# Kernel tuning notes

Measured on AMD Instinct MI355X. Metric: run time of the kernel, lower is better.

Reference implementation:

```python
import jax, jax.numpy as jnp
import numpy as np

T, D_IN, N_RES, D_OUT = 8192, 64, 2048, 64
SPECTRAL_RADIUS = 0.95


def setup_inputs() -> dict:
    key = jax.random.key(0)
    k1, k2, k3, k4, k5 = jax.random.split(key, 5)
    u = jax.random.normal(k1, (T, D_IN), dtype=jnp.float32)
    W_in = jax.random.normal(k2, (N_RES, D_IN), dtype=jnp.float32) * 0.1
    W = jax.random.normal(k3, (N_RES, N_RES), dtype=jnp.float32)
    # Spectral-radius rescale exactly as in __init__: max |Re(eigvals)|
    max_eig = float(np.max(np.abs(np.linalg.eigvals(np.asarray(W)).real)))
    W = W * (SPECTRAL_RADIUS / max_eig)
    W_out = jax.random.normal(k4, (D_OUT, N_RES), dtype=jnp.float32) * (1.0 / np.sqrt(N_RES))
    b_out = jax.random.normal(k5, (D_OUT,), dtype=jnp.float32) * 0.01
    return {"u": u, "W_in": W_in, "W": W, "W_out": W_out, "b_out": b_out}


def reference(u, W_in, W, W_out, b_out):
    # x_t = tanh(W_in @ u_t + W @ x_{t-1}); y_t = W_out @ x_t + b
    # Precompute input projections for all timesteps in one GEMM.
    inp_proj = u @ W_in.T  # (T, N_RES)

    def step(x, proj_t):
        x_new = jnp.tanh(proj_t + W @ x)
        return x_new, x_new

    x0 = jnp.zeros((N_RES,), dtype=u.dtype)
    _, states = jax.lax.scan(step, x0, inp_proj)  # states: (T, N_RES)
    outputs = states @ W_out.T + b_out            # (T, D_OUT)
    return outputs
```

## Files before the change

kernel.cpp:

```cpp
#include <hip/hip_runtime.h>

#define T_STEPS 8192
#define NRES    2048
#define DIN     64
#define DOUT    64

typedef unsigned long long u64;
typedef unsigned int u32;


__global__ __launch_bounds__(256) void esn_init_ring(u64* __restrict__ ring) {
  int idx = blockIdx.x * 256 + threadIdx.x;
  if (idx < 3 * NRES) ring[idx] = 0ull;
}

__global__ __launch_bounds__(256) void esn_transpose(const float* __restrict__ Wout,
                                                     float* __restrict__ WT) {
  int idx = blockIdx.x * 256 + threadIdx.x;
  int d = idx >> 11;
  int k = idx & (NRES - 1);
  WT[k * DOUT + d] = Wout[idx];
}

__global__ __launch_bounds__(256) void esn_scan(const float* __restrict__ u,
                                                const float* __restrict__ Win,
                                                const float* __restrict__ W,
                                                float* __restrict__ states,
                                                u64* __restrict__ ring) {
  const int tid  = threadIdx.x;
  const int lane = tid & 63;
  const int wv   = tid >> 6;
  const int blk  = blockIdx.x;
  const int r0   = blk * 8 + wv * 2;
  const int r1   = r0 + 1;

  __shared__ float xs[NRES];

  float w0[32], w1[32];
#pragma unroll
  for (int g = 0; g < 8; ++g) {
    const float4 a = *(const float4*)(W + (size_t)r0 * NRES + g * 256 + lane * 4);
    w0[g * 4 + 0] = a.x; w0[g * 4 + 1] = a.y; w0[g * 4 + 2] = a.z; w0[g * 4 + 3] = a.w;
    const float4 c = *(const float4*)(W + (size_t)r1 * NRES + g * 256 + lane * 4);
    w1[g * 4 + 0] = c.x; w1[g * 4 + 1] = c.y; w1[g * 4 + 2] = c.z; w1[g * 4 + 3] = c.w;
  }
  const float win0 = Win[r0 * DIN + lane];
  const float win1 = Win[r1 * DIN + lane];

  for (int t = 0; t < T_STEPS; ++t) {
    __syncthreads();
    if (t == 0) {
#pragma unroll
      for (int j = 0; j < 8; ++j) xs[j * 256 + tid] = 0.0f;
    } else {
      const u64* rb  = ring + ((t + 2) % 3) * NRES;
      const u32 want = (u32)t;
      u64 v[8];
#pragma unroll
      for (int j = 0; j < 8; ++j)
        v[j] = __hip_atomic_load(rb + j * 256 + tid, __ATOMIC_RELAXED,
                                 __HIP_MEMORY_SCOPE_AGENT);
      for (;;) {
        bool ok = true;
#pragma unroll
        for (int j = 0; j < 8; ++j) ok = ok && ((u32)v[j] == want);
        if (ok) break;
#pragma unroll
        for (int j = 0; j < 8; ++j)
          if ((u32)v[j] != want)
            v[j] = __hip_atomic_load(rb + j * 256 + tid, __ATOMIC_RELAXED,
                                     __HIP_MEMORY_SCOPE_AGENT);
      }
#pragma unroll
      for (int j = 0; j < 8; ++j)
        xs[j * 256 + tid] = __uint_as_float((u32)(v[j] >> 32));
    }
    __syncthreads();

    const float uv = u[t * DIN + lane];
    float a0 = win0 * uv;
    float a1 = win1 * uv;
#pragma unroll
    for (int g = 0; g < 8; ++g) {
      const float4 xv = *(const float4*)(xs + g * 256 + lane * 4);
      a0 = fmaf(w0[g * 4 + 0], xv.x, a0);
      a0 = fmaf(w0[g * 4 + 1], xv.y, a0);
      a0 = fmaf(w0[g * 4 + 2], xv.z, a0);
      a0 = fmaf(w0[g * 4 + 3], xv.w, a0);
      a1 = fmaf(w1[g * 4 + 0], xv.x, a1);
      a1 = fmaf(w1[g * 4 + 1], xv.y, a1);
      a1 = fmaf(w1[g * 4 + 2], xv.z, a1);
      a1 = fmaf(w1[g * 4 + 3], xv.w, a1);
    }
#pragma unroll
    for (int off = 32; off > 0; off >>= 1) {
      a0 += __shfl_xor(a0, off, 64);
      a1 += __shfl_xor(a1, off, 64);
    }
    if (lane < 2) {
      const float s  = (lane == 0) ? a0 : a1;
      const float xv = tanhf(s);
      const int r    = r0 + lane;
      states[(size_t)t * NRES + r] = xv;
      const u64 word = ((u64)__float_as_uint(xv) << 32) | (u32)(t + 1);
      __hip_atomic_store(ring + (t % 3) * NRES + r, word, __ATOMIC_RELAXED,
                         __HIP_MEMORY_SCOPE_AGENT);
    }
  }
}

__global__ __launch_bounds__(256) void esn_out_gemm(const float* __restrict__ states,
                                                    const float* __restrict__ WT,
                                                    const float* __restrict__ bout,
                                                    float* __restrict__ out) {
  const int tid  = threadIdx.x;
  const int lane = tid & 63;
  const int grp  = tid >> 6;
  const int t0   = blockIdx.x * 16 + grp * 4;

  float acc0 = 0.f, acc1 = 0.f, acc2 = 0.f, acc3 = 0.f;
  const float* s0 = states + (size_t)(t0 + 0) * NRES;
  const float* s1 = states + (size_t)(t0 + 1) * NRES;
  const float* s2 = states + (size_t)(t0 + 2) * NRES;
  const float* s3 = states + (size_t)(t0 + 3) * NRES;

  for (int k = 0; k < NRES; k += 4) {
    const float4 a = *(const float4*)(s0 + k);
    const float4 b = *(const float4*)(s1 + k);
    const float4 c = *(const float4*)(s2 + k);
    const float4 d = *(const float4*)(s3 + k);
    const float wA = WT[(k + 0) * DOUT + lane];
    const float wB = WT[(k + 1) * DOUT + lane];
    const float wC = WT[(k + 2) * DOUT + lane];
    const float wD = WT[(k + 3) * DOUT + lane];
    acc0 = fmaf(a.x, wA, acc0); acc0 = fmaf(a.y, wB, acc0);
    acc0 = fmaf(a.z, wC, acc0); acc0 = fmaf(a.w, wD, acc0);
    acc1 = fmaf(b.x, wA, acc1); acc1 = fmaf(b.y, wB, acc1);
    acc1 = fmaf(b.z, wC, acc1); acc1 = fmaf(b.w, wD, acc1);
    acc2 = fmaf(c.x, wA, acc2); acc2 = fmaf(c.y, wB, acc2);
    acc2 = fmaf(c.z, wC, acc2); acc2 = fmaf(c.w, wD, acc2);
    acc3 = fmaf(d.x, wA, acc3); acc3 = fmaf(d.y, wB, acc3);
    acc3 = fmaf(d.z, wC, acc3); acc3 = fmaf(d.w, wD, acc3);
  }
  const float bb = bout[lane];
  out[(size_t)(t0 + 0) * DOUT + lane] = acc0 + bb;
  out[(size_t)(t0 + 1) * DOUT + lane] = acc1 + bb;
  out[(size_t)(t0 + 2) * DOUT + lane] = acc2 + bb;
  out[(size_t)(t0 + 3) * DOUT + lane] = acc3 + bb;
}

extern "C" void kernel_launch(void* const* d_in, const int* in_sizes, int n_in,
                              void* d_out, int out_size, void* d_ws, size_t ws_size,
                              hipStream_t stream) {
  const float* u    = (const float*)d_in[0];
  const float* Win  = (const float*)d_in[1];
  const float* W    = (const float*)d_in[2];
  const float* Wout = (const float*)d_in[3];
  const float* bout = (const float*)d_in[4];
  float* out = (float*)d_out;

  char* ws = (char*)d_ws;
  float* states = (float*)ws;
  u64*   ring   = (u64*)(ws + (size_t)T_STEPS * NRES * sizeof(float));
  float* WT     = (float*)(ws + (size_t)T_STEPS * NRES * sizeof(float)
                              + (size_t)3 * NRES * sizeof(u64));

  hipLaunchKernelGGL(esn_init_ring, dim3(24), dim3(256), 0, stream, ring);
  hipLaunchKernelGGL(esn_transpose, dim3((DOUT * NRES) / 256), dim3(256), 0, stream,
                     Wout, WT);
  hipLaunchKernelGGL(esn_scan, dim3(256), dim3(256), 0, stream,
                     u, Win, W, states, ring);
  hipLaunchKernelGGL(esn_out_gemm, dim3(T_STEPS / 16), dim3(256), 0, stream,
                     states, WT, bout, out);
}
```

Measured before the change: 23.40 ms.

## Pack two state values per ring word using NaN sentinels instead of step tags

Changes the cross-block handoff ring from one value plus a step tag per 64-bit word to two float values per word. A quiet-NaN pattern marks empty slots, and a 4-deep ring lets each producer clear the slot for a future step after writing. This halves the number of atomic loads each thread polls per step and the volume of synchronisation traffic. The u load is also hoisted ahead of the spin loop. It relies on tanh never producing NaN and on the clear-ahead ordering staying correct with relaxed atomics.

```diff
diff --git a/kernel.cpp b/kernel.cpp
--- a/kernel.cpp
+++ b/kernel.cpp
@@ -8,10 +8,12 @@
 typedef unsigned long long u64;
 typedef unsigned int u32;
 
+#define QNAN_PAIR 0x7FC000007FC00000ull
+
 
 __global__ __launch_bounds__(256) void esn_init_ring(u64* __restrict__ ring) {
   int idx = blockIdx.x * 256 + threadIdx.x;
-  if (idx < 3 * NRES) ring[idx] = 0ull;
+  if (idx < 4 * NRES / 2) ring[idx] = QNAN_PAIR;
 }
 
 __global__ __launch_bounds__(256) void esn_transpose(const float* __restrict__ Wout,
@@ -49,35 +51,45 @@
 
   for (int t = 0; t < T_STEPS; ++t) {
     __syncthreads();
+    float uv;
     if (t == 0) {
 #pragma unroll
       for (int j = 0; j < 8; ++j) xs[j * 256 + tid] = 0.0f;
+      uv = u[t * DIN + lane];
     } else {
-      const u64* rb  = ring + ((t + 2) % 3) * NRES;
-      const u32 want = (u32)t;
-      u64 v[8];
+      u64* rb = ring + ((t + 3) & 3) * (NRES / 2);
+      u64 v[4];
 #pragma unroll
-      for (int j = 0; j < 8; ++j)
+      for (int j = 0; j < 4; ++j)
         v[j] = __hip_atomic_load(rb + j * 256 + tid, __ATOMIC_RELAXED,
                                  __HIP_MEMORY_SCOPE_AGENT);
+      uv = u[t * DIN + lane];
       for (;;) {
         bool ok = true;
 #pragma unroll
-        for (int j = 0; j < 8; ++j) ok = ok && ((u32)v[j] == want);
+        for (int j = 0; j < 4; ++j) {
+          const float lo = __uint_as_float((u32)v[j]);
+          const float hi = __uint_as_float((u32)(v[j] >> 32));
+          ok = ok && (lo == lo) && (hi == hi);
+        }
         if (ok) break;
 #pragma unroll
-        for (int j = 0; j < 8; ++j)
-          if ((u32)v[j] != want)
+        for (int j = 0; j < 4; ++j) {
+          const float lo = __uint_as_float((u32)v[j]);
+          const float hi = __uint_as_float((u32)(v[j] >> 32));
+          if (!(lo == lo) || !(hi == hi))
             v[j] = __hip_atomic_load(rb + j * 256 + tid, __ATOMIC_RELAXED,
                                      __HIP_MEMORY_SCOPE_AGENT);
+        }
       }
 #pragma unroll
-      for (int j = 0; j < 8; ++j)
-        xs[j * 256 + tid] = __uint_as_float((u32)(v[j] >> 32));
+      for (int j = 0; j < 4; ++j) {
+        xs[j * 512 + 2 * tid + 0] = __uint_as_float((u32)v[j]);
+        xs[j * 512 + 2 * tid + 1] = __uint_as_float((u32)(v[j] >> 32));
+      }
     }
     __syncthreads();
 
-    const float uv = u[t * DIN + lane];
     float a0 = win0 * uv;
     float a1 = win1 * uv;
 #pragma unroll
@@ -97,14 +109,15 @@
       a0 += __shfl_xor(a0, off, 64);
       a1 += __shfl_xor(a1, off, 64);
     }
-    if (lane < 2) {
-      const float s  = (lane == 0) ? a0 : a1;
-      const float xv = tanhf(s);
-      const int r    = r0 + lane;
-      states[(size_t)t * NRES + r] = xv;
-      const u64 word = ((u64)__float_as_uint(xv) << 32) | (u32)(t + 1);
-      __hip_atomic_store(ring + (t % 3) * NRES + r, word, __ATOMIC_RELAXED,
-                         __HIP_MEMORY_SCOPE_AGENT);
+    const float x0 = tanhf(a0);
+    const float x1 = tanhf(a1);
+    if (lane == 0) {
+      const u64 word = ((u64)__float_as_uint(x1) << 32) | (u64)__float_as_uint(x0);
+      __hip_atomic_store(ring + (t & 3) * (NRES / 2) + (r0 >> 1), word,
+                         __ATOMIC_RELAXED, __HIP_MEMORY_SCOPE_AGENT);
+      __hip_atomic_store(ring + ((t + 1) & 3) * (NRES / 2) + (r0 >> 1), QNAN_PAIR,
+                         __ATOMIC_RELAXED, __HIP_MEMORY_SCOPE_AGENT);
+      *(u64*)(states + (size_t)t * NRES + r0) = word;
     }
   }
 }
@@ -163,9 +176,9 @@
   float* states = (float*)ws;
   u64*   ring   = (u64*)(ws + (size_t)T_STEPS * NRES * sizeof(float));
   float* WT     = (float*)(ws + (size_t)T_STEPS * NRES * sizeof(float)
-                              + (size_t)3 * NRES * sizeof(u64));
+                              + (size_t)4 * NRES * sizeof(float));
 
-  hipLaunchKernelGGL(esn_init_ring, dim3(24), dim3(256), 0, stream, ring);
+  hipLaunchKernelGGL(esn_init_ring, dim3(16), dim3(256), 0, stream, ring);
   hipLaunchKernelGGL(esn_transpose, dim3((DOUT * NRES) / 256), dim3(256), 0, stream,
                      Wout, WT);
   hipLaunchKernelGGL(esn_scan, dim3(256), dim3(256), 0, stream,
```

Result: slower. 27.74 ms (+18.5%).

## Use one row per wave, 512-thread blocks, double-buffered LDS to drop a barrier

Applied to the files above, without the earlier changes.

The persistent scan kernel now gives each wave a single reservoir row and runs 512-thread blocks, so each block still owns 8 rows but has twice as many threads polling the ring. The shared state vector is double-buffered by timestep parity, which removes the leading __syncthreads per step. Each ring element is written to LDS as soon as its flag matches, rather than after all elements are ready. The trade-offs are more waves per CU, half the FMA work per wave, and a doubled LDS footprint.

```diff
diff --git a/kernel.cpp b/kernel.cpp
--- a/kernel.cpp
+++ b/kernel.cpp
@@ -9,8 +9,8 @@
 typedef unsigned int u32;
 
 
-__global__ __launch_bounds__(256) void esn_init_ring(u64* __restrict__ ring) {
-  int idx = blockIdx.x * 256 + threadIdx.x;
+__global__ __launch_bounds__(512) void esn_init_ring(u64* __restrict__ ring) {
+  int idx = blockIdx.x * 512 + threadIdx.x;
   if (idx < 3 * NRES) ring[idx] = 0ull;
 }
 
@@ -22,7 +22,7 @@
   WT[k * DOUT + d] = Wout[idx];
 }
 
-__global__ __launch_bounds__(256) void esn_scan(const float* __restrict__ u,
+__global__ __launch_bounds__(512) void esn_scan(const float* __restrict__ u,
                                                 const float* __restrict__ Win,
                                                 const float* __restrict__ W,
                                                 float* __restrict__ states,
@@ -30,79 +30,66 @@
   const int tid  = threadIdx.x;
   const int lane = tid & 63;
   const int wv   = tid >> 6;
-  const int blk  = blockIdx.x;
-  const int r0   = blk * 8 + wv * 2;
-  const int r1   = r0 + 1;
+  const int r    = blockIdx.x * 8 + wv;
 
-  __shared__ float xs[NRES];
+  __shared__ float xs[2][NRES];
 
-  float w0[32], w1[32];
+  float wr[32];
 #pragma unroll
   for (int g = 0; g < 8; ++g) {
-    const float4 a = *(const float4*)(W + (size_t)r0 * NRES + g * 256 + lane * 4);
-    w0[g * 4 + 0] = a.x; w0[g * 4 + 1] = a.y; w0[g * 4 + 2] = a.z; w0[g * 4 + 3] = a.w;
-    const float4 c = *(const float4*)(W + (size_t)r1 * NRES + g * 256 + lane * 4);
-    w1[g * 4 + 0] = c.x; w1[g * 4 + 1] = c.y; w1[g * 4 + 2] = c.z; w1[g * 4 + 3] = c.w;
+    const float4 a = *(const float4*)(W + (size_t)r * NRES + g * 256 + lane * 4);
+    wr[g * 4 + 0] = a.x; wr[g * 4 + 1] = a.y;
+    wr[g * 4 + 2] = a.z; wr[g * 4 + 3] = a.w;
   }
-  const float win0 = Win[r0 * DIN + lane];
-  const float win1 = Win[r1 * DIN + lane];
+  const float win = Win[r * DIN + lane];
 
   for (int t = 0; t < T_STEPS; ++t) {
-    __syncthreads();
+    const float uv = u[t * DIN + lane];
+    float* xb = xs[t & 1];
     if (t == 0) {
 #pragma unroll
-      for (int j = 0; j < 8; ++j) xs[j * 256 + tid] = 0.0f;
+      for (int j = 0; j < 4; ++j) xb[j * 512 + tid] = 0.0f;
     } else {
       const u64* rb  = ring + ((t + 2) % 3) * NRES;
       const u32 want = (u32)t;
-      u64 v[8];
+      u64 v[4];
 #pragma unroll
-      for (int j = 0; j < 8; ++j)
-        v[j] = __hip_atomic_load(rb + j * 256 + tid, __ATOMIC_RELAXED,
+      for (int j = 0; j < 4; ++j)
+        v[j] = __hip_atomic_load(rb + j * 512 + tid, __ATOMIC_RELAXED,
                                  __HIP_MEMORY_SCOPE_AGENT);
-      for (;;) {
-        bool ok = true;
+      u32 pend = 0xFu;
+      while (pend) {
 #pragma unroll
-        for (int j = 0; j < 8; ++j) ok = ok && ((u32)v[j] == want);
-        if (ok) break;
-#pragma unroll
-        for (int j = 0; j < 8; ++j)
-          if ((u32)v[j] != want)
-            v[j] = __hip_atomic_load(rb + j * 256 + tid, __ATOMIC_RELAXED,
-                                     __HIP_MEMORY_SCOPE_AGENT);
+        for (int j = 0; j < 4; ++j) {
+          if (pend & (1u << j)) {
+            if ((u32)v[j] == want) {
+              xb[j * 512 + tid] = __uint_as_float((u32)(v[j] >> 32));
+              pend &= ~(1u << j);
+            } else {
+              v[j] = __hip_atomic_load(rb + j * 512 + tid, __ATOMIC_RELAXED,
+                                       __HIP_MEMORY_SCOPE_AGENT);
+            }
+          }
+        }
       }
-#pragma unroll
-      for (int j = 0; j < 8; ++j)
-        xs[j * 256 + tid] = __uint_as_float((u32)(v[j] >> 32));
     }
     __syncthreads();
 
-    const float uv = u[t * DIN + lane];
-    float a0 = win0 * uv;
-    float a1 = win1 * uv;
+    float acc = win * uv;
 #pragma unroll
     for (int g = 0; g < 8; ++g) {
-      const float4 xv = *(const float4*)(xs + g * 256 + lane * 4);
-      a0 = fmaf(w0[g * 4 + 0], xv.x, a0);
-      a0 = fmaf(w0[g * 4 + 1], xv.y, a0);
-      a0 = fmaf(w0[g * 4 + 2], xv.z, a0);
-      a0 = fmaf(w0[g * 4 + 3], xv.w, a0);
-      a1 = fmaf(w1[g * 4 + 0], xv.x, a1);
-      a1 = fmaf(w1[g * 4 + 1], xv.y, a1);
-      a1 = fmaf(w1[g * 4 + 2], xv.z, a1);
-      a1 = fmaf(w1[g * 4 + 3], xv.w, a1);
+      const float4 xv = *(const float4*)(xb + g * 256 + lane * 4);
+      acc = fmaf(wr[g * 4 + 0], xv.x, acc);
+      acc = fmaf(wr[g * 4 + 1], xv.y, acc);
+      acc = fmaf(wr[g * 4 + 2], xv.z, acc);
+      acc = fmaf(wr[g * 4 + 3], xv.w, acc);
     }
 #pragma unroll
-    for (int off = 32; off > 0; off >>= 1) {
-      a0 += __shfl_xor(a0, off, 64);
-      a1 += __shfl_xor(a1, off, 64);
-    }
-    if (lane < 2) {
-      const float s  = (lane == 0) ? a0 : a1;
-      const float xv = tanhf(s);
-      const int r    = r0 + lane;
-      states[(size_t)t * NRES + r] = xv;
-      const u64 word = ((u64)__float_as_uint(xv) << 32) | (u32)(t + 1);
+    for (int off = 32; off > 0; off >>= 1) acc += __shfl_xor(acc, off, 64);
+    const float x = tanhf(acc);
+    if (lane == 0) {
+      states[(size_t)t * NRES + r] = x;
+      const u64 word = ((u64)__float_as_uint(x) << 32) | (u32)(t + 1);
       __hip_atomic_store(ring + (t % 3) * NRES + r, word, __ATOMIC_RELAXED,
                          __HIP_MEMORY_SCOPE_AGENT);
     }
@@ -165,10 +152,10 @@
   float* WT     = (float*)(ws + (size_t)T_STEPS * NRES * sizeof(float)
                               + (size_t)3 * NRES * sizeof(u64));
 
-  hipLaunchKernelGGL(esn_init_ring, dim3(24), dim3(256), 0, stream, ring);
+  hipLaunchKernelGGL(esn_init_ring, dim3(12), dim3(512), 0, stream, ring);
   hipLaunchKernelGGL(esn_transpose, dim3((DOUT * NRES) / 256), dim3(256), 0, stream,
                      Wout, WT);
-  hipLaunchKernelGGL(esn_scan, dim3(256), dim3(256), 0, stream,
+  hipLaunchKernelGGL(esn_scan, dim3(256), dim3(512), 0, stream,
                      u, Win, W, states, ring);
   hipLaunchKernelGGL(esn_out_gemm, dim3(T_STEPS / 16), dim3(256), 0, stream,
                      states, WT, bout, out);
```

Result: slower. 38.59 ms (+64.9%).
